# Performance work log

Measured on AMD Instinct MI355X. Metric: run time of the kernel, lower is better.

Reference implementation:

```python
import jax, jax.numpy as jnp
import numpy as np

N, E, NFEAT, NHID, NCLASS = 50000, 800000, 8, 128, 112
SMOOTH = 0.5          # smoo init arg
NEG_SLOPE_ATT = 0.2   # LeakyReLU slope inside sparse attention (SpGAT convention)
NEG_SLOPE_OUT = 0.01  # F.leaky_relu default in the outer loop
EPS = 1e-16


def setup_inputs() -> dict:
    key = jax.random.key(0)
    ks = jax.random.split(key, 12)
    g = lambda k, shape, s=0.1: jax.random.normal(k, shape, dtype=jnp.float32) * s
    return {
        "x": jax.random.normal(ks[0], (N, NFEAT), dtype=jnp.float32),
        "edge_index": jax.random.randint(ks[1], (2, E), 0, N, dtype=jnp.int64) if jax.config.jax_enable_x64 else jax.random.randint(ks[1], (2, E), 0, N, dtype=jnp.int32),
        "edge_weight": jax.random.uniform(ks[2], (E,), dtype=jnp.float32),
        # ScattterAttentionLayer 1: nfeat -> nhid (weight W, attention vector a split into src/dst halves)
        "W1": g(ks[3], (NFEAT, NHID)),
        "a1_src": g(ks[4], (NHID,)),
        "a1_dst": g(ks[5], (NHID,)),
        # ScattterAttentionLayer 2: nhid -> nhid
        "W2": g(ks[6], (NHID, NHID)),
        "a2_src": g(ks[7], (NHID,)),
        "a2_dst": g(ks[8], (NHID,)),
        # shared BatchNorm1d(nhid)
        "gamma": jnp.ones((NHID,), jnp.float32),
        "beta": jnp.zeros((NHID,), jnp.float32),
        # GC_withres: nhid -> nclass
        "Wg": g(ks[9], (NHID, NCLASS)),
        "bg": jnp.zeros((NCLASS,), jnp.float32),
    }


def scatter_attention(h_in, W, a_src, a_dst, src, dst):
    """Sparse GAT-style scatter attention (SpGraphAttentionLayer math).
    score_ij = exp(-leakyrelu(a_src.h_i + a_dst.h_j)); softmax-normalized per dst node."""
    h = h_in @ W                                   # [N, F]
    f_src = h @ a_src                              # [N]
    f_dst = h @ a_dst                              # [N]
    e = jnp.exp(-jax.nn.leaky_relu(f_src[src] + f_dst[dst], NEG_SLOPE_ATT))  # [E]
    denom = jax.ops.segment_sum(e, dst, num_segments=N) + EPS                # [N]
    num = jax.ops.segment_sum(e[:, None] * h[src], dst, num_segments=N)      # [N, F]
    return num / denom[:, None]


def batchnorm(x, gamma, beta):
    mu = x.mean(axis=0)
    var = x.var(axis=0)
    return (x - mu) * jax.lax.rsqrt(var + 1e-5) * gamma + beta


def reference(x, edge_index, edge_weight, W1, a1_src, a1_dst, W2, a2_src, a2_dst, gamma, beta, Wg, bg):
    src, dst = edge_index[0], edge_index[1]
    # conv loop (nlayers=3 -> two ScattterAttentionLayer convs), shared bn1, leaky_relu; dropout=identity (eval)
    h = scatter_attention(x, W1, a1_src, a1_dst, src, dst)
    h = jax.nn.leaky_relu(batchnorm(h, gamma, beta), NEG_SLOPE_OUT)
    h = scatter_attention(h, W2, a2_src, a2_dst, src, dst)
    h = jax.nn.leaky_relu(batchnorm(h, gamma, beta), NEG_SLOPE_OUT)
    # GC_withres: spmm((smooth*A + I)/(1+smooth), h @ Wg) + bias
    support = h @ Wg                               # [N, nclass]
    w = (SMOOTH / (1.0 + SMOOTH)) * edge_weight    # [E]
    agg = jax.ops.segment_sum(w[:, None] * support[src], dst, num_segments=N)
    return agg + support / (1.0 + SMOOTH) + bg
```

## Files before the change

### kernel.cpp

```cpp
#include <hip/hip_runtime.h>
#include <hip/hip_bf16.h>

#define N_NODES 50000
#define N_EDGES 800000
#define NFEAT   8
#define NHID    128
#define NCLASS  112
#define SEG_EPS 1e-16f
#define BN_EPS  1e-5f
#define CAP     64
#define MACRO_TILES 782
#define STAT_ROWS 50
#define STAT_BLOCKS 1000
#define NODE_RANGE 6250
#define FILL_CHUNK 2048
#define FILL_CHUNKS 391

typedef __hip_bfloat16 bf16;
typedef __attribute__((ext_vector_type(8))) short short8;
typedef __attribute__((ext_vector_type(4))) float f32x4;

__device__ __forceinline__ float bfbits2f(unsigned int lo16) {
    union { unsigned int u; float f; } c; c.u = lo16 << 16; return c.f;
}

__global__ __launch_bounds__(256)
void k_fill_bucket(const int* __restrict__ src, const int* __restrict__ dst,
                   const float* __restrict__ ewt,
                   int* __restrict__ cnt, unsigned int* __restrict__ bucket) {
    const int range = blockIdx.x & 7;
    const int chunk = blockIdx.x >> 3;
    const int lo = range * NODE_RANGE, hi = lo + NODE_RANGE;
    const int e0 = chunk * FILL_CHUNK + threadIdx.x;
#pragma unroll
    for (int i = 0; i < 8; i++) {
        int e = e0 + i * 256;
        if (e >= N_EDGES) break;
        int d = dst[e];
        if (d < lo || d >= hi) continue;
        int slot = atomicAdd(&cnt[d], 1);
        if (slot < CAP) {
            unsigned int iw = (unsigned int)(ewt[e] * 32767.f + 0.5f);
            bucket[d * CAP + slot] = ((unsigned int)src[e] << 15) | iw;
        }
    }
}

__global__ __launch_bounds__(256)
void k_sort_bucket(const int* __restrict__ cnt, unsigned int* __restrict__ bucket) {
    int d = blockIdx.x * 4 + (threadIdx.x >> 6);
    int lane = threadIdx.x & 63;
    int deg = min(cnt[d], CAP);
    unsigned int v = (lane < deg) ? bucket[d * CAP + lane] : 0xFFFFFFFFu;
#pragma unroll
    for (int k = 2; k <= 64; k <<= 1) {
#pragma unroll
        for (int s = k >> 1; s > 0; s >>= 1) {
            unsigned int o = (unsigned int)__shfl_xor((int)v, s);
            bool keepmin = ((lane & s) == 0) == ((lane & k) == 0);
            v = keepmin ? min(v, o) : max(v, o);
        }
    }
    if (lane < deg) bucket[d * CAP + lane] = v;
}

__global__ void k_w1proj(const float* __restrict__ W1,
                         const float* __restrict__ a1s, const float* __restrict__ a1d,
                         float* __restrict__ w1s, float* __restrict__ w1d) {
    int w = threadIdx.x >> 6, lane = threadIdx.x & 63;
    int k = w & 7;
    const float* a = (w < 8) ? a1s : a1d;
    float v = W1[k * NHID + lane] * a[lane] + W1[k * NHID + 64 + lane] * a[64 + lane];
#pragma unroll
    for (int off = 32; off > 0; off >>= 1) v += __shfl_down(v, off);
    if (lane == 0) ((w < 8) ? w1s : w1d)[k] = v;
}

__global__ void k_fsfd(const float* __restrict__ x,
                       const float* __restrict__ w1s, const float* __restrict__ w1d,
                       float* __restrict__ fs, float* __restrict__ fd) {
    int i = blockIdx.x * 256 + threadIdx.x;
    if (i >= N_NODES) return;
    const float4 x0 = ((const float4*)x)[i * 2];
    const float4 x1 = ((const float4*)x)[i * 2 + 1];
    fs[i] = x0.x*w1s[0] + x0.y*w1s[1] + x0.z*w1s[2] + x0.w*w1s[3]
          + x1.x*w1s[4] + x1.y*w1s[5] + x1.z*w1s[6] + x1.w*w1s[7];
    fd[i] = x0.x*w1d[0] + x0.y*w1d[1] + x0.z*w1d[2] + x0.w*w1d[3]
          + x1.x*w1d[4] + x1.y*w1d[5] + x1.z*w1d[6] + x1.w*w1d[7];
}

__global__ void k_gather_x(const int* __restrict__ cnt, const unsigned int* __restrict__ bucket,
                           const float* __restrict__ fs, const float* __restrict__ fd,
                           const float* __restrict__ x, float* __restrict__ xaggn) {
    int d = blockIdx.x * 4 + (threadIdx.x >> 6);
    int lane = threadIdx.x & 63;
    int col = lane & 7, eslot = lane >> 3;
    int dg = min(cnt[d], CAP);
    float fdd = fd[d];
    float acc = 0.f, den = 0.f;
    for (int base = 0; base < dg; base += 8) {
        int e = base + eslot;
        if (e < dg) {
            int s = bucket[d * CAP + e] >> 15;
            float f = fs[s] + fdd;
            float lr = f > 0.f ? f : 0.2f * f;
            float c = __expf(-lr);
            den += c;
            acc += c * x[s * NFEAT + col];
        }
    }
#pragma unroll
    for (int off = 8; off < 64; off <<= 1) {
        acc += __shfl_xor(acc, off);
        den += __shfl_xor(den, off);
    }
    if (eslot == 0) xaggn[d * NFEAT + col] = acc / (den + SEG_EPS);
}

__global__ __launch_bounds__(256)
void k_y1_gemm(const float* __restrict__ xaggn, const float* __restrict__ W1,
               bf16* __restrict__ y1, float* __restrict__ Psum, float* __restrict__ Psq) {
    int t = threadIdx.x;
    int r = t >> 7, j = t & 127;
    float w[NFEAT];
#pragma unroll
    for (int k = 0; k < NFEAT; k++) w[k] = W1[k * NHID + j];
    float ls = 0.f, lq = 0.f;
    for (int row = blockIdx.x * 2 + r; row < N_NODES; row += gridDim.x * 2) {
        const float4 x0 = ((const float4*)xaggn)[row * 2];
        const float4 x1 = ((const float4*)xaggn)[row * 2 + 1];
        float v = x0.x*w[0] + x0.y*w[1] + x0.z*w[2] + x0.w*w[3]
                + x1.x*w[4] + x1.y*w[5] + x1.z*w[6] + x1.w*w[7];
        y1[(size_t)row * NHID + j] = __float2bfloat16(v);
        ls += v; lq += v * v;
    }
    __shared__ float sbuf[256];
    sbuf[t] = ls; __syncthreads();
    if (r == 0) Psum[blockIdx.x * 128 + j] = sbuf[j] + sbuf[j + 128];
    __syncthreads();
    sbuf[t] = lq; __syncthreads();
    if (r == 0) Psq[blockIdx.x * 128 + j] = sbuf[j] + sbuf[j + 128];
}

__global__ __launch_bounds__(128)
void k_bn_stats_part(const bf16* __restrict__ y,
                     float* __restrict__ Psum, float* __restrict__ Psq) {
    int j = threadIdx.x;
    int i0 = blockIdx.x * STAT_ROWS;
    float ls = 0.f, lq = 0.f;
    for (int i = i0; i < i0 + STAT_ROWS; i++) {
        float v = __bfloat162float(y[(size_t)i * NHID + j]);
        ls += v; lq += v * v;
    }
    Psum[blockIdx.x * 128 + j] = ls;
    Psq[blockIdx.x * 128 + j] = lq;
}

__global__ __launch_bounds__(256)
void k_reduce_a(const float* __restrict__ Psum, const float* __restrict__ Psq,
                int nIn, int chunk,
                float* __restrict__ Qsum, float* __restrict__ Qsq) {
    int j = threadIdx.x & 127;
    int h = threadIdx.x >> 7;
    int u = blockIdx.x * 2 + h;
    int b0 = u * chunk, b1 = min(b0 + chunk, nIn);
    float s = 0.f, q = 0.f;
#pragma unroll 8
    for (int b = b0; b < b1; b++) {
        s += Psum[b * 128 + j];
        q += Psq[b * 128 + j];
    }
    Qsum[u * 128 + j] = s;
    Qsq[u * 128 + j] = q;
}

__global__ __launch_bounds__(512)
void k_reduce_b(const float* __restrict__ Qsum, const float* __restrict__ Qsq,
                const float* __restrict__ gamma, const float* __restrict__ beta,
                float* __restrict__ scale, float* __restrict__ shift) {
    int j = threadIdx.x & 127;
    int g = threadIdx.x >> 7;
    float s = 0.f, q = 0.f;
#pragma unroll
    for (int u = g * 8; u < g * 8 + 8; u++) {
        s += Qsum[u * 128 + j];
        q += Qsq[u * 128 + j];
    }
    __shared__ float Ls[4][128], Lq[4][128];
    Ls[g][j] = s; Lq[g][j] = q;
    __syncthreads();
    if (g == 0) {
        float st = ((Ls[0][j] + Ls[1][j]) + Ls[2][j]) + Ls[3][j];
        float qt = ((Lq[0][j] + Lq[1][j]) + Lq[2][j]) + Lq[3][j];
        float mu = st * (1.f / N_NODES);
        float var = qt * (1.f / N_NODES) - mu * mu;
        float rs = rsqrtf(var + BN_EPS);
        float ga = gamma[j];
        scale[j] = rs * ga;
        shift[j] = beta[j] - mu * rs * ga;
    }
}

__global__ void k_w2proj(const float* __restrict__ W2,
                         const float* __restrict__ as_, const float* __restrict__ ad_,
                         float* __restrict__ ws_, float* __restrict__ wd_) {
    int k = blockIdx.x, n = threadIdx.x;
    float w = W2[k * NHID + n];
    float vs = w * as_[n], vd = w * ad_[n];
#pragma unroll
    for (int off = 32; off > 0; off >>= 1) { vs += __shfl_down(vs, off); vd += __shfl_down(vd, off); }
    __shared__ float ps[2], pd[2];
    if ((n & 63) == 0) { ps[n >> 6] = vs; pd[n >> 6] = vd; }
    __syncthreads();
    if (n == 0) { ws_[k] = ps[0] + ps[1]; wd_[k] = pd[0] + pd[1]; }
}

template<int NCV, bool ATT>
__global__ __launch_bounds__(256)
void k_gemm_mfma(const bf16* __restrict__ Yin,
                 const float* __restrict__ scale, const float* __restrict__ shift,
                 const float* __restrict__ W,
                 bf16* __restrict__ hout,
                 const float* __restrict__ w2s, const float* __restrict__ w2d,
                 float* __restrict__ fs, float* __restrict__ fd) {
    constexpr int NT = NCV / 16;
    __shared__ bf16 Wt[128 * 136];
    __shared__ bf16 At[64 * 136];
    const int t = threadIdx.x;
    for (int idx = t; idx < 128 * NCV; idx += 256) {
        int k = idx / NCV, n = idx - k * NCV;
        Wt[n * 136 + k] = __float2bfloat16(W[idx]);
    }
    const int p  = t & 63;
    const int rg = t >> 6;
    const float sc0 = scale[2*p],   sh0 = shift[2*p];
    const float sc1 = scale[2*p+1], sh1 = shift[2*p+1];
    float ws0, ws1, wd0, wd1;
    if (ATT) { ws0 = w2s[2*p]; ws1 = w2s[2*p+1]; wd0 = w2d[2*p]; wd1 = w2d[2*p+1]; }
    const int lane = t & 63;
    const int m16 = lane & 15;
    const int g = lane >> 4;
    __syncthreads();

    for (int mt = blockIdx.x; mt < MACRO_TILES; mt += gridDim.x) {
        const int row0 = mt * 64;
#pragma unroll
        for (int i2 = 0; i2 < 16; i2++) {
            int row = rg + i2 * 4;
            int grow = row0 + row;
            unsigned int u = (grow < N_NODES) ? ((const unsigned int*)Yin)[(size_t)grow * 64 + p] : 0u;
            float v0 = bfbits2f(u & 0xFFFF) * sc0 + sh0; v0 = v0 > 0.f ? v0 : 0.01f * v0;
            float v1 = bfbits2f(u >> 16)    * sc1 + sh1; v1 = v1 > 0.f ? v1 : 0.01f * v1;
            union { unsigned int u; bf16 b[2]; } pk;
            pk.b[0] = __float2bfloat16(v0);
            pk.b[1] = __float2bfloat16(v1);
            *(unsigned int*)&At[row * 136 + 2 * p] = pk.u;
            if (ATT) {
                float vs = v0 * ws0 + v1 * ws1;
                float vd = v0 * wd0 + v1 * wd1;
#pragma unroll
                for (int off = 32; off > 0; off >>= 1) {
                    vs += __shfl_xor(vs, off);
                    vd += __shfl_xor(vd, off);
                }
                if (p == 0 && grow < N_NODES) { fs[grow] = vs; fd[grow] = vd; }
            }
        }
        __syncthreads();
        f32x4 acc[NT];
#pragma unroll
        for (int c = 0; c < NT; c++) acc[c] = (f32x4){0.f, 0.f, 0.f, 0.f};
#pragma unroll
        for (int kk = 0; kk < 4; kk++) {
            short8 af = *(const short8*)&At[(rg * 16 + m16) * 136 + kk * 32 + g * 8];
#pragma unroll
            for (int c = 0; c < NT; c++) {
                short8 bfr = *(const short8*)&Wt[(c * 16 + m16) * 136 + kk * 32 + g * 8];
                acc[c] = __builtin_amdgcn_mfma_f32_16x16x32_bf16(af, bfr, acc[c], 0, 0, 0);
            }
        }
        const int orow = row0 + rg * 16 + g * 4;
#pragma unroll
        for (int c = 0; c < NT; c++) {
#pragma unroll
            for (int r = 0; r < 4; r++) {
                int grow = orow + r;
                if (grow < N_NODES)
                    hout[(size_t)grow * NCV + c * 16 + m16] = __float2bfloat16(acc[c][r]);
            }
        }
        __syncthreads();
    }
}

__global__ __launch_bounds__(256)
void k_gather_attn_bf(const int* __restrict__ cnt, const unsigned int* __restrict__ bucket,
                      const float* __restrict__ fs, const float* __restrict__ fd,
                      const bf16* __restrict__ h, bf16* __restrict__ y) {
    int q = threadIdx.x >> 6;
    int j = threadIdx.x & 63;
    int d = blockIdx.x * 4 + q;
    __shared__ int s_idx[4][CAP];
    __shared__ float s_e[4][CAP];
    int deg = min(cnt[d], CAP);
    float fdd = fd[d];
    if (j < deg) {
        int s = bucket[d * CAP + j] >> 15;
        float f = fs[s] + fdd;
        float lr = f > 0.f ? f : 0.2f * f;
        s_idx[q][j] = s;
        s_e[q][j] = __expf(-lr);
    }
    __syncthreads();
    float n0 = 0.f, n1 = 0.f, den = 0.f;
#pragma unroll 4
    for (int k = 0; k < deg; k++) {
        float e = s_e[q][k];
        unsigned int u = *(const unsigned int*)&h[(size_t)s_idx[q][k] * NHID + 2 * j];
        den += e;
        n0 += e * bfbits2f(u & 0xFFFF);
        n1 += e * bfbits2f(u >> 16);
    }
    float rs = 1.f / (den + SEG_EPS);
    union { unsigned int u; bf16 b[2]; } pk;
    pk.b[0] = __float2bfloat16(n0 * rs);
    pk.b[1] = __float2bfloat16(n1 * rs);
    ((unsigned int*)y)[(size_t)d * 64 + j] = pk.u;
}

__global__ __launch_bounds__(256)
void k_gather_out_bf(const int* __restrict__ cnt, const unsigned int* __restrict__ bucket,
                     const bf16* __restrict__ sup, const float* __restrict__ bg,
                     float* __restrict__ out) {
    int q = threadIdx.x >> 6;
    int j = threadIdx.x & 63;
    int d = blockIdx.x * 4 + q;
    __shared__ int s_idx[4][CAP];
    __shared__ float s_w[4][CAP];
    int deg = min(cnt[d], CAP);
    if (j < deg) {
        unsigned int b = bucket[d * CAP + j];
        s_idx[q][j] = b >> 15;
        s_w[q][j] = (float)(b & 0x7FFF) * (1.f / (32767.f * 3.f));
    }
    __syncthreads();
    if (j >= NCLASS / 2) return;
    float a0 = 0.f, a1 = 0.f;
#pragma unroll 4
    for (int k = 0; k < deg; k++) {
        float w = s_w[q][k];
        unsigned int u = *(const unsigned int*)&sup[(size_t)s_idx[q][k] * NCLASS + 2 * j];
        a0 += w * bfbits2f(u & 0xFFFF);
        a1 += w * bfbits2f(u >> 16);
    }
    unsigned int us = *(const unsigned int*)&sup[(size_t)d * NCLASS + 2 * j];
    float2 o;
    o.x = a0 + bfbits2f(us & 0xFFFF) * (2.f / 3.f) + bg[2 * j];
    o.y = a1 + bfbits2f(us >> 16)    * (2.f / 3.f) + bg[2 * j + 1];
    *(float2*)&out[(size_t)d * NCLASS + 2 * j] = o;
}

extern "C" void kernel_launch(void* const* d_in, const int* in_sizes, int n_in,
                              void* d_out, int out_size, void* d_ws, size_t ws_size,
                              hipStream_t stream) {
    const float* x    = (const float*)d_in[0];
    const int*   ei   = (const int*)d_in[1];
    const float* ewt  = (const float*)d_in[2];
    const float* W1   = (const float*)d_in[3];
    const float* a1s  = (const float*)d_in[4];
    const float* a1d  = (const float*)d_in[5];
    const float* W2   = (const float*)d_in[6];
    const float* a2s  = (const float*)d_in[7];
    const float* a2d  = (const float*)d_in[8];
    const float* gam  = (const float*)d_in[9];
    const float* bet  = (const float*)d_in[10];
    const float* Wg   = (const float*)d_in[11];
    const float* bg   = (const float*)d_in[12];
    float* out = (float*)d_out;

    const int* src = ei;
    const int* dst = ei + N_EDGES;

    float* ws    = (float*)d_ws;
    bf16*  Yb    = (bf16*)ws;
    bf16*  Hb    = (bf16*)(ws + 3203072);
    unsigned int* bucket = (unsigned int*)(ws + 6403072);
    float* xagg  = ws + 9603072;
    float* fs    = ws + 10003072;
    float* fd    = ws + 10053072;
    int*   cnt   = (int*)(ws + 10103072);
    float* scale = ws + 10153072;
    float* shift = scale + 128;
    float* w1s   = shift + 128;
    float* w1d   = w1s + 8;
    float* w2s   = w1d + 8;
    float* w2d   = w2s + 128;
    float* Psum  = ws + 10153600;
    float* Psq   = Psum + 128000;
    float* Qsum  = Psq + 128000;
    float* Qsq   = Qsum + 4096;

    hipMemsetAsync(cnt, 0, (size_t)N_NODES * 4, stream);
    k_fill_bucket<<<FILL_CHUNKS * 8, 256, 0, stream>>>(src, dst, ewt, cnt, bucket);
    k_sort_bucket<<<N_NODES / 4, 256, 0, stream>>>(cnt, bucket);

    k_w1proj<<<1, 1024, 0, stream>>>(W1, a1s, a1d, w1s, w1d);
    k_fsfd<<<(N_NODES + 255) / 256, 256, 0, stream>>>(x, w1s, w1d, fs, fd);
    k_gather_x<<<N_NODES / 4, 256, 0, stream>>>(cnt, bucket, fs, fd, x, xagg);
    k_y1_gemm<<<256, 256, 0, stream>>>(xagg, W1, Yb, Psum, Psq);
    k_reduce_a<<<16, 256, 0, stream>>>(Psum, Psq, 256, 8, Qsum, Qsq);
    k_reduce_b<<<1, 512, 0, stream>>>(Qsum, Qsq, gam, bet, scale, shift);

    k_w2proj<<<128, 128, 0, stream>>>(W2, a2s, a2d, w2s, w2d);
    k_gemm_mfma<128, true><<<MACRO_TILES, 256, 0, stream>>>(Yb, scale, shift, W2, Hb,
                                                            w2s, w2d, fs, fd);
    k_gather_attn_bf<<<N_NODES / 4, 256, 0, stream>>>(cnt, bucket, fs, fd, Hb, Yb);
    k_bn_stats_part<<<STAT_BLOCKS, 128, 0, stream>>>(Yb, Psum, Psq);
    k_reduce_a<<<16, 256, 0, stream>>>(Psum, Psq, STAT_BLOCKS, 32, Qsum, Qsq);
    k_reduce_b<<<1, 512, 0, stream>>>(Qsum, Qsq, gam, bet, scale, shift);

    k_gemm_mfma<112, false><<<MACRO_TILES, 256, 0, stream>>>(Yb, scale, shift, Wg, Hb,
                                                             nullptr, nullptr, nullptr, nullptr);
    k_gather_out_bf<<<N_NODES / 4, 256, 0, stream>>>(cnt, bucket, Hb, bg, out);
}
```

Measured before the change: 331.0 us.

## Fuse preprocessing, BN statistics and attention projections into neighbouring kernels

The bucket sort moves into the first-layer gather, which takes edge indices from registers by shuffle. The W1 attention projection moves into the fs/fd kernel, and the first BatchNorm reduction becomes one block. The second layer's BN sum and sum-of-squares are now computed inside the attention gather, which processes four node groups per block, so the separate stats pass over Y is gone. The fs/fd projections for layer 2 use an extra MFMA against bf16-packed attention vectors instead of wave shuffles, and the edge fill loads destination indices with vector loads. This removes several launches and a full re-read of Y. In exchange it lowers the precision of the layer-2 attention logits to bf16 inputs and relies on wave-local LDS ordering without a barrier.

```diff
diff --git a/kernel.cpp b/kernel.cpp
--- a/kernel.cpp
+++ b/kernel.cpp
@@ -10,11 +10,12 @@
 #define BN_EPS  1e-5f
 #define CAP     64
 #define MACRO_TILES 782
-#define STAT_ROWS 50
-#define STAT_BLOCKS 1000
 #define NODE_RANGE 6250
 #define FILL_CHUNK 2048
 #define FILL_CHUNKS 391
+#define ATTN_BLOCKS 3125
+#define ATTN_ITERS 4
+#define Y1_BLOCKS 256
 
 typedef __hip_bfloat16 bf16;
 typedef __attribute__((ext_vector_type(8))) short short8;
@@ -22,6 +23,13 @@
 
 __device__ __forceinline__ float bfbits2f(unsigned int lo16) {
     union { unsigned int u; float f; } c; c.u = lo16 << 16; return c.f;
+}
+
+__device__ __forceinline__ unsigned int pack_bf2(float a, float b) {
+    union { unsigned int u; bf16 h[2]; } t;
+    t.h[0] = __float2bfloat16(a);
+    t.h[1] = __float2bfloat16(b);
+    return t.u;
 }
 
 __global__ __launch_bounds__(256)
@@ -31,13 +39,16 @@
     const int range = blockIdx.x & 7;
     const int chunk = blockIdx.x >> 3;
     const int lo = range * NODE_RANGE, hi = lo + NODE_RANGE;
-    const int e0 = chunk * FILL_CHUNK + threadIdx.x;
+    const int e0 = chunk * FILL_CHUNK + threadIdx.x * 8;
+    if (e0 >= N_EDGES) return;
+    const int4 d0 = *(const int4*)&dst[e0];
+    const int4 d1 = *(const int4*)&dst[e0 + 4];
+    const int dd[8] = {d0.x, d0.y, d0.z, d0.w, d1.x, d1.y, d1.z, d1.w};
 #pragma unroll
     for (int i = 0; i < 8; i++) {
-        int e = e0 + i * 256;
-        if (e >= N_EDGES) break;
-        int d = dst[e];
+        int d = dd[i];
         if (d < lo || d >= hi) continue;
+        int e = e0 + i;
         int slot = atomicAdd(&cnt[d], 1);
         if (slot < CAP) {
             unsigned int iw = (unsigned int)(ewt[e] * 32767.f + 0.5f);
@@ -47,10 +58,40 @@
 }
 
 __global__ __launch_bounds__(256)
-void k_sort_bucket(const int* __restrict__ cnt, unsigned int* __restrict__ bucket) {
-    int d = blockIdx.x * 4 + (threadIdx.x >> 6);
-    int lane = threadIdx.x & 63;
-    int deg = min(cnt[d], CAP);
+void k_fsfd(const float* __restrict__ x, const float* __restrict__ W1,
+            const float* __restrict__ a1s, const float* __restrict__ a1d,
+            float* __restrict__ fs, float* __restrict__ fd) {
+    __shared__ float sw[16];
+    const int t = threadIdx.x, w = t >> 6, lane = t & 63;
+#pragma unroll
+    for (int dd = 0; dd < 4; dd++) {
+        int dot = w + dd * 4;
+        int k = dot & 7;
+        const float* a = (dot < 8) ? a1s : a1d;
+        float v = W1[k * NHID + lane] * a[lane] + W1[k * NHID + 64 + lane] * a[64 + lane];
+#pragma unroll
+        for (int off = 32; off > 0; off >>= 1) v += __shfl_down(v, off);
+        if (lane == 0) sw[dot] = v;
+    }
+    __syncthreads();
+    const int i = blockIdx.x * 256 + t;
+    if (i < N_NODES) {
+        const float4 x0 = ((const float4*)x)[i * 2];
+        const float4 x1 = ((const float4*)x)[i * 2 + 1];
+        fs[i] = x0.x*sw[0] + x0.y*sw[1] + x0.z*sw[2] + x0.w*sw[3]
+              + x1.x*sw[4] + x1.y*sw[5] + x1.z*sw[6] + x1.w*sw[7];
+        fd[i] = x0.x*sw[8] + x0.y*sw[9] + x0.z*sw[10] + x0.w*sw[11]
+              + x1.x*sw[12] + x1.y*sw[13] + x1.z*sw[14] + x1.w*sw[15];
+    }
+}
+
+__global__ __launch_bounds__(256)
+void k_sort_gather_x(const int* __restrict__ cnt, unsigned int* __restrict__ bucket,
+                     const float* __restrict__ fs, const float* __restrict__ fd,
+                     const float* __restrict__ x, float* __restrict__ xaggn) {
+    const int d = blockIdx.x * 4 + (threadIdx.x >> 6);
+    const int lane = threadIdx.x & 63;
+    const int deg = min(cnt[d], CAP);
     unsigned int v = (lane < deg) ? bucket[d * CAP + lane] : 0xFFFFFFFFu;
 #pragma unroll
     for (int k = 2; k <= 64; k <<= 1) {
@@ -62,46 +103,14 @@
         }
     }
     if (lane < deg) bucket[d * CAP + lane] = v;
-}
-
-__global__ void k_w1proj(const float* __restrict__ W1,
-                         const float* __restrict__ a1s, const float* __restrict__ a1d,
-                         float* __restrict__ w1s, float* __restrict__ w1d) {
-    int w = threadIdx.x >> 6, lane = threadIdx.x & 63;
-    int k = w & 7;
-    const float* a = (w < 8) ? a1s : a1d;
-    float v = W1[k * NHID + lane] * a[lane] + W1[k * NHID + 64 + lane] * a[64 + lane];
-#pragma unroll
-    for (int off = 32; off > 0; off >>= 1) v += __shfl_down(v, off);
-    if (lane == 0) ((w < 8) ? w1s : w1d)[k] = v;
-}
-
-__global__ void k_fsfd(const float* __restrict__ x,
-                       const float* __restrict__ w1s, const float* __restrict__ w1d,
-                       float* __restrict__ fs, float* __restrict__ fd) {
-    int i = blockIdx.x * 256 + threadIdx.x;
-    if (i >= N_NODES) return;
-    const float4 x0 = ((const float4*)x)[i * 2];
-    const float4 x1 = ((const float4*)x)[i * 2 + 1];
-    fs[i] = x0.x*w1s[0] + x0.y*w1s[1] + x0.z*w1s[2] + x0.w*w1s[3]
-          + x1.x*w1s[4] + x1.y*w1s[5] + x1.z*w1s[6] + x1.w*w1s[7];
-    fd[i] = x0.x*w1d[0] + x0.y*w1d[1] + x0.z*w1d[2] + x0.w*w1d[3]
-          + x1.x*w1d[4] + x1.y*w1d[5] + x1.z*w1d[6] + x1.w*w1d[7];
-}
-
-__global__ void k_gather_x(const int* __restrict__ cnt, const unsigned int* __restrict__ bucket,
-                           const float* __restrict__ fs, const float* __restrict__ fd,
-                           const float* __restrict__ x, float* __restrict__ xaggn) {
-    int d = blockIdx.x * 4 + (threadIdx.x >> 6);
-    int lane = threadIdx.x & 63;
-    int col = lane & 7, eslot = lane >> 3;
-    int dg = min(cnt[d], CAP);
-    float fdd = fd[d];
+    const int col = lane & 7, eslot = lane >> 3;
+    const float fdd = fd[d];
     float acc = 0.f, den = 0.f;
-    for (int base = 0; base < dg; base += 8) {
+    for (int base = 0; base < deg; base += 8) {
         int e = base + eslot;
-        if (e < dg) {
-            int s = bucket[d * CAP + e] >> 15;
+        unsigned int u = (unsigned int)__shfl((int)v, e);
+        if (e < deg) {
+            int s = u >> 15;
             float f = fs[s] + fdd;
             float lr = f > 0.f ? f : 0.2f * f;
             float c = __expf(-lr);
@@ -142,18 +151,31 @@
     if (r == 0) Psq[blockIdx.x * 128 + j] = sbuf[j] + sbuf[j + 128];
 }
 
-__global__ __launch_bounds__(128)
-void k_bn_stats_part(const bf16* __restrict__ y,
-                     float* __restrict__ Psum, float* __restrict__ Psq) {
-    int j = threadIdx.x;
-    int i0 = blockIdx.x * STAT_ROWS;
-    float ls = 0.f, lq = 0.f;
-    for (int i = i0; i < i0 + STAT_ROWS; i++) {
-        float v = __bfloat162float(y[(size_t)i * NHID + j]);
-        ls += v; lq += v * v;
-    }
-    Psum[blockIdx.x * 128 + j] = ls;
-    Psq[blockIdx.x * 128 + j] = lq;
+__global__ __launch_bounds__(512)
+void k_reduce_full(const float* __restrict__ Psum, const float* __restrict__ Psq,
+                   const float* __restrict__ gamma, const float* __restrict__ beta,
+                   float* __restrict__ scale, float* __restrict__ shift) {
+    int j = threadIdx.x & 127;
+    int g = threadIdx.x >> 7;
+    float s = 0.f, q = 0.f;
+#pragma unroll 8
+    for (int b = g * 64; b < g * 64 + 64; b++) {
+        s += Psum[b * 128 + j];
+        q += Psq[b * 128 + j];
+    }
+    __shared__ float Ls[4][128], Lq[4][128];
+    Ls[g][j] = s; Lq[g][j] = q;
+    __syncthreads();
+    if (g == 0) {
+        float st = ((Ls[0][j] + Ls[1][j]) + Ls[2][j]) + Ls[3][j];
+        float qt = ((Lq[0][j] + Lq[1][j]) + Lq[2][j]) + Lq[3][j];
+        float mu = st * (1.f / N_NODES);
+        float var = qt * (1.f / N_NODES) - mu * mu;
+        float rs = rsqrtf(var + BN_EPS);
+        float ga = gamma[j];
+        scale[j] = rs * ga;
+        shift[j] = beta[j] - mu * rs * ga;
+    }
 }
 
 __global__ __launch_bounds__(256)
@@ -224,7 +246,7 @@
                  const float* __restrict__ w2s, const float* __restrict__ w2d,
                  float* __restrict__ fs, float* __restrict__ fd) {
     constexpr int NT = NCV / 16;
-    __shared__ bf16 Wt[128 * 136];
+    __shared__ bf16 Wt[NCV * 136];
     __shared__ bf16 At[64 * 136];
     const int t = threadIdx.x;
     for (int idx = t; idx < 128 * NCV; idx += 256) {
@@ -235,11 +257,28 @@
     const int rg = t >> 6;
     const float sc0 = scale[2*p],   sh0 = shift[2*p];
     const float sc1 = scale[2*p+1], sh1 = shift[2*p+1];
-    float ws0, ws1, wd0, wd1;
-    if (ATT) { ws0 = w2s[2*p]; ws1 = w2s[2*p+1]; wd0 = w2d[2*p]; wd1 = w2d[2*p+1]; }
     const int lane = t & 63;
     const int m16 = lane & 15;
     const int g = lane >> 4;
+    short8 attb[4];
+    if constexpr (ATT) {
+#pragma unroll
+        for (int kk = 0; kk < 4; kk++) {
+            union { short8 s; unsigned int u[4]; } pk;
+            if (m16 < 2) {
+                const float* wv = (m16 == 0) ? w2s : w2d;
+                const float4 f0 = *(const float4*)&wv[kk * 32 + g * 8];
+                const float4 f1 = *(const float4*)&wv[kk * 32 + g * 8 + 4];
+                pk.u[0] = pack_bf2(f0.x, f0.y);
+                pk.u[1] = pack_bf2(f0.z, f0.w);
+                pk.u[2] = pack_bf2(f1.x, f1.y);
+                pk.u[3] = pack_bf2(f1.z, f1.w);
+            } else {
+                pk.u[0] = pk.u[1] = pk.u[2] = pk.u[3] = 0u;
+            }
+            attb[kk] = pk.s;
+        }
+    }
     __syncthreads();
 
     for (int mt = blockIdx.x; mt < MACRO_TILES; mt += gridDim.x) {
@@ -251,25 +290,13 @@
             unsigned int u = (grow < N_NODES) ? ((const unsigned int*)Yin)[(size_t)grow * 64 + p] : 0u;
             float v0 = bfbits2f(u & 0xFFFF) * sc0 + sh0; v0 = v0 > 0.f ? v0 : 0.01f * v0;
             float v1 = bfbits2f(u >> 16)    * sc1 + sh1; v1 = v1 > 0.f ? v1 : 0.01f * v1;
-            union { unsigned int u; bf16 b[2]; } pk;
-            pk.b[0] = __float2bfloat16(v0);
-            pk.b[1] = __float2bfloat16(v1);
-            *(unsigned int*)&At[row * 136 + 2 * p] = pk.u;
-            if (ATT) {
-                float vs = v0 * ws0 + v1 * ws1;
-                float vd = v0 * wd0 + v1 * wd1;
-#pragma unroll
-                for (int off = 32; off > 0; off >>= 1) {
-                    vs += __shfl_xor(vs, off);
-                    vd += __shfl_xor(vd, off);
-                }
-                if (p == 0 && grow < N_NODES) { fs[grow] = vs; fd[grow] = vd; }
-            }
+            *(unsigned int*)&At[row * 136 + 2 * p] = pack_bf2(v0, v1);
         }
         __syncthreads();
         f32x4 acc[NT];
 #pragma unroll
         for (int c = 0; c < NT; c++) acc[c] = (f32x4){0.f, 0.f, 0.f, 0.f};
+        f32x4 accA = (f32x4){0.f, 0.f, 0.f, 0.f};
 #pragma unroll
         for (int kk = 0; kk < 4; kk++) {
             short8 af = *(const short8*)&At[(rg * 16 + m16) * 136 + kk * 32 + g * 8];
@@ -278,6 +305,8 @@
                 short8 bfr = *(const short8*)&Wt[(c * 16 + m16) * 136 + kk * 32 + g * 8];
                 acc[c] = __builtin_amdgcn_mfma_f32_16x16x32_bf16(af, bfr, acc[c], 0, 0, 0);
             }
+            if constexpr (ATT)
+                accA = __builtin_amdgcn_mfma_f32_16x16x32_bf16(af, attb[kk], accA, 0, 0, 0);
         }
         const int orow = row0 + rg * 16 + g * 4;
 #pragma unroll
@@ -289,6 +318,16 @@
                     hout[(size_t)grow * NCV + c * 16 + m16] = __float2bfloat16(acc[c][r]);
             }
         }
+        if constexpr (ATT) {
+            if (m16 < 2) {
+                float* o = (m16 == 0) ? fs : fd;
+#pragma unroll
+                for (int r = 0; r < 4; r++) {
+                    int grow = orow + r;
+                    if (grow < N_NODES) o[grow] = accA[r];
+                }
+            }
+        }
         __syncthreads();
     }
 }
@@ -296,36 +335,57 @@
 __global__ __launch_bounds__(256)
 void k_gather_attn_bf(const int* __restrict__ cnt, const unsigned int* __restrict__ bucket,
                       const float* __restrict__ fs, const float* __restrict__ fd,
-                      const bf16* __restrict__ h, bf16* __restrict__ y) {
-    int q = threadIdx.x >> 6;
-    int j = threadIdx.x & 63;
-    int d = blockIdx.x * 4 + q;
+                      const bf16* __restrict__ h, bf16* __restrict__ y,
+                      float* __restrict__ Psum, float* __restrict__ Psq) {
+    const int q = threadIdx.x >> 6;
+    const int j = threadIdx.x & 63;
     __shared__ int s_idx[4][CAP];
     __shared__ float s_e[4][CAP];
-    int deg = min(cnt[d], CAP);
-    float fdd = fd[d];
-    if (j < deg) {
-        int s = bucket[d * CAP + j] >> 15;
-        float f = fs[s] + fdd;
-        float lr = f > 0.f ? f : 0.2f * f;
-        s_idx[q][j] = s;
-        s_e[q][j] = __expf(-lr);
-    }
-    __syncthreads();
-    float n0 = 0.f, n1 = 0.f, den = 0.f;
+    __shared__ float red[4][64][2];
+    float ls0 = 0.f, ls1 = 0.f, lq0 = 0.f, lq1 = 0.f;
+    for (int it = 0; it < ATTN_ITERS; it++) {
+        const int d = (blockIdx.x + it * ATTN_BLOCKS) * 4 + q;
+        const int deg = min(cnt[d], CAP);
+        const float fdd = fd[d];
+        if (j < deg) {
+            int s = bucket[d * CAP + j] >> 15;
+            float f = fs[s] + fdd;
+            float lr = f > 0.f ? f : 0.2f * f;
+            s_idx[q][j] = s;
+            s_e[q][j] = __expf(-lr);
+        }
+        float n0 = 0.f, n1 = 0.f, den = 0.f;
 #pragma unroll 4
-    for (int k = 0; k < deg; k++) {
-        float e = s_e[q][k];
-        unsigned int u = *(const unsigned int*)&h[(size_t)s_idx[q][k] * NHID + 2 * j];
-        den += e;
-        n0 += e * bfbits2f(u & 0xFFFF);
-        n1 += e * bfbits2f(u >> 16);
-    }
-    float rs = 1.f / (den + SEG_EPS);
-    union { unsigned int u; bf16 b[2]; } pk;
-    pk.b[0] = __float2bfloat16(n0 * rs);
-    pk.b[1] = __float2bfloat16(n1 * rs);
-    ((unsigned int*)y)[(size_t)d * 64 + j] = pk.u;
+        for (int k = 0; k < deg; k++) {
+            float e = s_e[q][k];
+            unsigned int u = *(const unsigned int*)&h[(size_t)s_idx[q][k] * NHID + 2 * j];
+            den += e;
+            n0 += e * bfbits2f(u & 0xFFFF);
+            n1 += e * bfbits2f(u >> 16);
+        }
+        float rsd = 1.f / (den + SEG_EPS);
+        float v0 = n0 * rsd, v1 = n1 * rsd;
+        ((unsigned int*)y)[(size_t)d * 64 + j] = pack_bf2(v0, v1);
+        ls0 += v0; lq0 += v0 * v0;
+        ls1 += v1; lq1 += v1 * v1;
+    }
+    red[q][j][0] = ls0; red[q][j][1] = ls1;
+    __syncthreads();
+    if (q == 0) {
+        float a0 = ((red[0][j][0] + red[1][j][0]) + red[2][j][0]) + red[3][j][0];
+        float a1 = ((red[0][j][1] + red[1][j][1]) + red[2][j][1]) + red[3][j][1];
+        Psum[blockIdx.x * 128 + 2 * j]     = a0;
+        Psum[blockIdx.x * 128 + 2 * j + 1] = a1;
+    }
+    __syncthreads();
+    red[q][j][0] = lq0; red[q][j][1] = lq1;
+    __syncthreads();
+    if (q == 0) {
+        float a0 = ((red[0][j][0] + red[1][j][0]) + red[2][j][0]) + red[3][j][0];
+        float a1 = ((red[0][j][1] + red[1][j][1]) + red[2][j][1]) + red[3][j][1];
+        Psq[blockIdx.x * 128 + 2 * j]     = a0;
+        Psq[blockIdx.x * 128 + 2 * j + 1] = a1;
+    }
 }
 
 __global__ __launch_bounds__(256)
@@ -391,32 +451,27 @@
     int*   cnt   = (int*)(ws + 10103072);
     float* scale = ws + 10153072;
     float* shift = scale + 128;
-    float* w1s   = shift + 128;
-    float* w1d   = w1s + 8;
-    float* w2s   = w1d + 8;
+    float* w2s   = shift + 128;
     float* w2d   = w2s + 128;
     float* Psum  = ws + 10153600;
-    float* Psq   = Psum + 128000;
-    float* Qsum  = Psq + 128000;
+    float* Psq   = Psum + 400000;
+    float* Qsum  = Psq + 400000;
     float* Qsq   = Qsum + 4096;
 
     hipMemsetAsync(cnt, 0, (size_t)N_NODES * 4, stream);
     k_fill_bucket<<<FILL_CHUNKS * 8, 256, 0, stream>>>(src, dst, ewt, cnt, bucket);
-    k_sort_bucket<<<N_NODES / 4, 256, 0, stream>>>(cnt, bucket);
-
-    k_w1proj<<<1, 1024, 0, stream>>>(W1, a1s, a1d, w1s, w1d);
-    k_fsfd<<<(N_NODES + 255) / 256, 256, 0, stream>>>(x, w1s, w1d, fs, fd);
-    k_gather_x<<<N_NODES / 4, 256, 0, stream>>>(cnt, bucket, fs, fd, x, xagg);
-    k_y1_gemm<<<256, 256, 0, stream>>>(xagg, W1, Yb, Psum, Psq);
-    k_reduce_a<<<16, 256, 0, stream>>>(Psum, Psq, 256, 8, Qsum, Qsq);
-    k_reduce_b<<<1, 512, 0, stream>>>(Qsum, Qsq, gam, bet, scale, shift);
+
+    k_fsfd<<<(N_NODES + 255) / 256, 256, 0, stream>>>(x, W1, a1s, a1d, fs, fd);
+    k_sort_gather_x<<<N_NODES / 4, 256, 0, stream>>>(cnt, bucket, fs, fd, x, xagg);
+    k_y1_gemm<<<Y1_BLOCKS, 256, 0, stream>>>(xagg, W1, Yb, Psum, Psq);
+    k_reduce_full<<<1, 512, 0, stream>>>(Psum, Psq, gam, bet, scale, shift);
 
     k_w2proj<<<128, 128, 0, stream>>>(W2, a2s, a2d, w2s, w2d);
     k_gemm_mfma<128, true><<<MACRO_TILES, 256, 0, stream>>>(Yb, scale, shift, W2, Hb,
                                                             w2s, w2d, fs, fd);
-    k_gather_attn_bf<<<N_NODES / 4, 256, 0, stream>>>(cnt, bucket, fs, fd, Hb, Yb);
-    k_bn_stats_part<<<STAT_BLOCKS, 128, 0, stream>>>(Yb, Psum, Psq);
-    k_reduce_a<<<16, 256, 0, stream>>>(Psum, Psq, STAT_BLOCKS, 32, Qsum, Qsq);
+    k_gather_attn_bf<<<ATTN_BLOCKS, 256, 0, stream>>>(cnt, bucket, fs, fd, Hb, Yb,
+                                                      Psum, Psq);
+    k_reduce_a<<<16, 256, 0, stream>>>(Psum, Psq, ATTN_BLOCKS, 98, Qsum, Qsq);
     k_reduce_b<<<1, 512, 0, stream>>>(Qsum, Qsq, gam, bet, scale, shift);
 
     k_gemm_mfma<112, false><<<MACRO_TILES, 256, 0, stream>>>(Yb, scale, shift, Wg, Hb,
```

Measured after the change: 323.7 us. 1.02x faster.
